# Kernel optimization log

Measured on AMD Instinct MI355X. Metric: run time of the kernel, lower is better.

Reference implementation:

```python
import jax, jax.numpy as jnp
import numpy as np
from jax import lax

SPLINE_ORDER = 3  # default in KANLinear


def make_grid(in_features, grid_size, order=SPLINE_ORDER):
    # grid_range = [-1, 1], extended by spline_order knots on each side
    h = 2.0 / grid_size
    g = jnp.arange(-order, grid_size + order + 1, dtype=jnp.float32) * h - 1.0
    return jnp.broadcast_to(g, (in_features, g.shape[0]))  # (in, G)


def b_splines(x, grid, order=SPLINE_ORDER):
    # x: (N, in), grid: (in, G). Cox-de Boor recursion.
    x = x[..., None]  # (N, in, 1)
    bases = ((x >= grid[:, :-1]) & (x < grid[:, 1:])).astype(x.dtype)
    for k in range(1, order + 1):
        bases = ((x - grid[:, : -(k + 1)]) / (grid[:, k:-1] - grid[:, : -(k + 1)]) * bases[..., :-1]
                 + (grid[:, k + 1:] - x) / (grid[:, k + 1:] - grid[:, 1:-k]) * bases[..., 1:])
    return bases  # (N, in, grid_size + order)


def kan_conv(x, base_w, spline_w, scaler, grid_size, kernel, pad):
    # x: (B, C, H, W); base_w: (n_convs, K); spline_w: (n_convs, K, grid_size+order); scaler: (n_convs, K)
    B, C, H, W = x.shape
    kh, kw = kernel
    K = kh * kw
    if K == 1:
        p = x.reshape(-1, 1)  # (B*C*H*W, 1)
        Ho, Wo = H, W
    else:
        # patches: (B, C*K, Ho, Wo), feature dim ordered channel-major then (kh, kw)
        patches = lax.conv_general_dilated_patches(x, (kh, kw), (1, 1), [(pad, pad), (pad, pad)])
        Ho, Wo = patches.shape[2], patches.shape[3]
        p = patches.reshape(B, C, K, Ho, Wo).transpose(0, 1, 3, 4, 2).reshape(-1, K)
    grid = make_grid(K, grid_size)
    bases = b_splines(p, grid)  # (N, K, coef) -- shared across all n_convs kernels
    base = jnp.einsum('ni,ki->nk', jax.nn.silu(p), base_w)
    spl = jnp.einsum('nic,kic->nk', bases, spline_w * scaler[..., None])
    n_convs = base_w.shape[0]
    # channel ordering: each input channel expanded into n_convs outputs (channel-major)
    out = (base + spl).reshape(B, C, Ho, Wo, n_convs).transpose(0, 1, 4, 2, 3)
    return out.reshape(B, C * n_convs, Ho, Wo)


def setup_inputs() -> dict:
    key = jax.random.key(0)
    ks = jax.random.split(key, 12)
    B, C, H, W = 4, 3, 256, 256
    coef3 = 3 + SPLINE_ORDER  # grid_size=3 -> 6 spline coefficients
    coef5 = 5 + SPLINE_ORDER  # grid_size=5 (default, kan_conv6) -> 8
    s9 = 1.0 / np.sqrt(9.0)
    return {
        'x': jax.random.normal(ks[0], (B, C, H, W), jnp.float32),
        'base_w1': jax.random.normal(ks[1], (2, 9), jnp.float32) * s9,
        'spline_w1': jax.random.normal(ks[2], (2, 9, coef3), jnp.float32) * 0.1,
        'scaler1': 1.0 + 0.1 * jax.random.normal(ks[3], (2, 9), jnp.float32),
        'base_w2': jax.random.normal(ks[4], (2, 9), jnp.float32) * s9,
        'spline_w2': jax.random.normal(ks[5], (2, 9, coef3), jnp.float32) * 0.1,
        'scaler2': 1.0 + 0.1 * jax.random.normal(ks[6], (2, 9), jnp.float32),
        'conv_w': jax.random.normal(ks[7], (3, 12, 1, 1), jnp.float32) * (1.0 / np.sqrt(12.0)),
        'conv_b': jax.random.normal(ks[8], (3,), jnp.float32) * 0.01,
        'base_w6': jax.random.normal(ks[9], (1, 1), jnp.float32),
        'spline_w6': jax.random.normal(ks[10], (1, 1, coef5), jnp.float32) * 0.1,
        'scaler6': 1.0 + 0.1 * jax.random.normal(ks[11], (1, 1), jnp.float32),
    }


def reference(x, base_w1, spline_w1, scaler1, base_w2, spline_w2, scaler2,
              conv_w, conv_b, base_w6, spline_w6, scaler6):
    x = kan_conv(x, base_w1, spline_w1, scaler1, grid_size=3, kernel=(3, 3), pad=1)   # (B,6,H,W)
    x = kan_conv(x, base_w2, spline_w2, scaler2, grid_size=3, kernel=(3, 3), pad=1)   # (B,12,H,W)
    x = jnp.einsum('bchw,oc->bohw', x, conv_w[:, :, 0, 0]) + conv_b[None, :, None, None]  # 1x1 conv -> (B,3,H,W)
    return kan_conv(x, base_w6, spline_w6, scaler6, grid_size=5, kernel=(1, 1), pad=0)  # (B,3,H,W)
```

## Files before the change

kernel.cpp:

```cpp
#include <hip/hip_runtime.h>
#include <hip/hip_fp16.h>

#define TILE 16
#define NT 768

typedef __fp16 h2f __attribute__((ext_vector_type(2)));

union H2U { h2f h; unsigned u; __half2 hh; };

__device__ __forceinline__ h2f u2h(unsigned u) { H2U t; t.u = u; return t.h; }

__device__ __forceinline__ unsigned pack_h2(float a, float b) {
    H2U t; t.hh = __halves2half2(__float2half_rn(a), __float2half_rn(b));
    return t.u;
}

__device__ __forceinline__ float fdot2(h2f a, h2f b, float acc) {
#if __has_builtin(__builtin_amdgcn_fdot2)
    return __builtin_amdgcn_fdot2(a, b, acc, false);
#else
    return acc + (float)a.x * (float)b.x + (float)a.y * (float)b.y;
#endif
}

struct Enc { float g, w; int si; };
__device__ __forceinline__ Enc kan_enc3(float v, float g0, float invh, float tmax) {
    Enc e;
    e.g = v / (1.0f + __expf(-v));
    float T = (v - g0) * invh;
    float U = (T >= 0.0f && T < tmax) ? T : -1.0f;
    float mf = floorf(U);
    e.w = U - mf;
    e.si = (int)mf + 1;
    return e;
}

__device__ __forceinline__ float poly_eval(float4 c, float w) {
    return ((c.w * w + c.z) * w + c.y) * w + c.x;
}

__device__ __forceinline__ float4 spline_poly(const float* __restrict__ sw, float sc,
                                              int ncoef, int si) {
    float4 v = make_float4(0.f, 0.f, 0.f, 0.f);
    if (si > 0) {
        int m = si - 1;
        float W[4];
        #pragma unroll
        for (int j = 0; j < 4; ++j) {
            int c = m - 3 + j;
            W[j] = (c >= 0 && c < ncoef) ? sw[c] * sc : 0.0f;
        }
        const float s6 = 1.0f / 6.0f;
        v.x = (W[0] + 4.0f * W[1] + W[2]) * s6;
        v.y = 3.0f * (W[2] - W[0]) * s6;
        v.z = (3.0f * W[0] - 6.0f * W[1] + 3.0f * W[2]) * s6;
        v.w = (W[3] - W[0] + 3.0f * (W[1] - W[2])) * s6;
    }
    return v;
}

__global__ __launch_bounds__(NT, 6) void ZS_MKAN_72121090834671_kernel(
    const float* __restrict__ x,
    const float* __restrict__ base_w1, const float* __restrict__ spline_w1,
    const float* __restrict__ scaler1,
    const float* __restrict__ base_w2, const float* __restrict__ spline_w2,
    const float* __restrict__ scaler2,
    const float* __restrict__ conv_w, const float* __restrict__ conv_b,
    const float* __restrict__ base_w6, const float* __restrict__ spline_w6,
    const float* __restrict__ scaler6,
    float* __restrict__ out)
{
    __shared__ float2  encXg[1200];
    __shared__ unsigned short encXs[1200];
    __shared__ float4  encYg[3][324];
    __shared__ ushort2 encYs[3][324];
    __shared__ uint4   coefH1[9][10];
    __shared__ uint4   coefH2[9][10];
    __shared__ float4  coef6[12];
    __shared__ float   sbw[2][18];
    __shared__ float   scw[36], scb[3];
    __shared__ float   sb6;
    __shared__ float   zpart[256][13];

    const int tid = threadIdx.x;
    const int tx0 = blockIdx.x * TILE;
    const int ty0 = blockIdx.y * TILE;
    const int b   = blockIdx.z;

    for (int e = tid; e < 180; e += NT) {
        int l = e / 90, r = e % 90, s = r / 10, si = r % 10;
        const float* sw  = l ? spline_w2 : spline_w1;
        const float* scl = l ? scaler2   : scaler1;
        float4 a = spline_poly(sw + s * 6,       scl[s],     6, si);
        float4 c = spline_poly(sw + (9 + s) * 6, scl[9 + s], 6, si);
        uint4 q;
        q.x = pack_h2(a.x, a.y); q.y = pack_h2(a.z, a.w);
        q.z = pack_h2(c.x, c.y); q.w = pack_h2(c.z, c.w);
        if (l) coefH2[s][si] = q; else coefH1[s][si] = q;
    }
    if (tid < 12) coef6[tid] = spline_poly(spline_w6, scaler6[0], 8, tid);
    if (tid < 18) { sbw[0][tid] = base_w1[tid]; sbw[1][tid] = base_w2[tid]; }
    if (tid < 36) scw[tid] = conv_w[tid];
    if (tid < 3)  scb[tid] = conv_b[tid];
    if (tid == 0) sb6 = base_w6[0];

    for (int i = tid; i < 1200; i += NT) {
        int c = i / 400, r = i % 400, ly = r / 20, lx = r % 20;
        int gy = ty0 - 2 + ly, gx = tx0 - 2 + lx;
        float v = 0.0f;
        if ((unsigned)gy < 256u && (unsigned)gx < 256u)
            v = x[((b * 3 + c) * 256 + gy) * 256 + gx];
        Enc e = kan_enc3(v, -3.0f, 1.5f, 9.0f);
        encXg[i] = make_float2(e.g, e.w);
        encXs[i] = (unsigned short)e.si;
    }
    __syncthreads();

    {
        float rb0[9], rb1[9];
        #pragma unroll
        for (int s = 0; s < 9; ++s) { rb0[s] = sbw[0][s]; rb1[s] = sbw[0][9 + s]; }
        for (int i = tid; i < 972; i += NT) {
            int c = i / 324, r = i % 324, ly = r / 18, lx = r % 18;
            float a0 = 0.0f, a1 = 0.0f;
            int base = c * 400 + ly * 20 + lx;
            #pragma unroll
            for (int s = 0; s < 9; ++s) {
                int p = base + (s / 3) * 20 + (s % 3);
                float2 gw = encXg[p];
                int si = encXs[p];
                uint4 q = coefH1[s][si];
                float w = gw.y, w2 = w * w;
                h2f p1 = __builtin_amdgcn_cvt_pkrtz(1.0f, w);
                h2f p2 = __builtin_amdgcn_cvt_pkrtz(w2, w2 * w);
                a0 += gw.x * rb0[s];
                a1 += gw.x * rb1[s];
                a0 = fdot2(u2h(q.x), p1, a0); a0 = fdot2(u2h(q.y), p2, a0);
                a1 = fdot2(u2h(q.z), p1, a1); a1 = fdot2(u2h(q.w), p2, a1);
            }
            int gy = ty0 - 1 + ly, gx = tx0 - 1 + lx;
            if (!((unsigned)gy < 256u && (unsigned)gx < 256u)) { a0 = 0.0f; a1 = 0.0f; }
            Enc e0 = kan_enc3(a0, -3.0f, 1.5f, 9.0f);
            Enc e1 = kan_enc3(a1, -3.0f, 1.5f, 9.0f);
            encYg[c][r] = make_float4(e0.g, e0.w, e1.g, e1.w);
            encYs[c][r] = make_ushort2((unsigned short)e0.si, (unsigned short)e1.si);
        }
    }
    __syncthreads();

    {
        const int pix = tid & 255;
        const int c   = tid >> 8;
        const int ly = pix >> 4, lx = pix & 15;
        float rb0[9], rb1[9];
        #pragma unroll
        for (int s = 0; s < 9; ++s) { rb0[s] = sbw[1][s]; rb1[s] = sbw[1][9 + s]; }
        const int rbase = ly * 18 + lx;
        float a00 = 0.0f, a01 = 0.0f, a10 = 0.0f, a11 = 0.0f;
        #pragma unroll
        for (int s = 0; s < 9; ++s) {
            int p = rbase + (s / 3) * 18 + (s % 3);
            float4 e = encYg[c][p];
            ushort2 ss = encYs[c][p];
            uint4 q0 = coefH2[s][ss.x];
            uint4 q1 = coefH2[s][ss.y];
            {
                float w = e.y, w2 = w * w;
                h2f p1 = __builtin_amdgcn_cvt_pkrtz(1.0f, w);
                h2f p2 = __builtin_amdgcn_cvt_pkrtz(w2, w2 * w);
                a00 += e.x * rb0[s];
                a01 += e.x * rb1[s];
                a00 = fdot2(u2h(q0.x), p1, a00); a00 = fdot2(u2h(q0.y), p2, a00);
                a01 = fdot2(u2h(q0.z), p1, a01); a01 = fdot2(u2h(q0.w), p2, a01);
            }
            {
                float w = e.w, w2 = w * w;
                h2f p1 = __builtin_amdgcn_cvt_pkrtz(1.0f, w);
                h2f p2 = __builtin_amdgcn_cvt_pkrtz(w2, w2 * w);
                a10 += e.z * rb0[s];
                a11 += e.z * rb1[s];
                a10 = fdot2(u2h(q1.x), p1, a10); a10 = fdot2(u2h(q1.y), p2, a10);
                a11 = fdot2(u2h(q1.z), p1, a11); a11 = fdot2(u2h(q1.w), p2, a11);
            }
        }
        zpart[pix][4 * c + 0] = a00;
        zpart[pix][4 * c + 1] = a01;
        zpart[pix][4 * c + 2] = a10;
        zpart[pix][4 * c + 3] = a11;
    }
    __syncthreads();

    if (tid < 256) {
        const int pix = tid;
        const int ly = pix >> 4, lx = pix & 15;
        const int gy = ty0 + ly, gx = tx0 + lx;
        float z[12];
        #pragma unroll
        for (int c = 0; c < 12; ++c) z[c] = zpart[pix][c];
        #pragma unroll
        for (int o = 0; o < 3; ++o) {
            float v = scb[o];
            #pragma unroll
            for (int c = 0; c < 12; ++c) v += scw[o * 12 + c] * z[c];
            Enc t = kan_enc3(v, -2.2f, 2.5f, 11.0f);
            out[((b * 3 + o) * 256 + gy) * 256 + gx] = t.g * sb6 + poly_eval(coef6[t.si], t.w);
        }
    }
}

extern "C" void kernel_launch(void* const* d_in, const int* in_sizes, int n_in,
                              void* d_out, int out_size, void* d_ws, size_t ws_size,
                              hipStream_t stream) {
    (void)in_sizes; (void)n_in; (void)d_ws; (void)ws_size; (void)out_size;
    const float* x         = (const float*)d_in[0];
    const float* base_w1   = (const float*)d_in[1];
    const float* spline_w1 = (const float*)d_in[2];
    const float* scaler1   = (const float*)d_in[3];
    const float* base_w2   = (const float*)d_in[4];
    const float* spline_w2 = (const float*)d_in[5];
    const float* scaler2   = (const float*)d_in[6];
    const float* conv_w    = (const float*)d_in[7];
    const float* conv_b    = (const float*)d_in[8];
    const float* base_w6   = (const float*)d_in[9];
    const float* spline_w6 = (const float*)d_in[10];
    const float* scaler6   = (const float*)d_in[11];
    float* out = (float*)d_out;

    dim3 grid(256 / TILE, 256 / TILE, 4);
    dim3 block(NT);
    ZS_MKAN_72121090834671_kernel<<<grid, block, 0, stream>>>(
        x, base_w1, spline_w1, scaler1, base_w2, spline_w2, scaler2,
        conv_w, conv_b, base_w6, spline_w6, scaler6, out);
}
```

Measured before the change: 24.00 us.

## Shrink block to 512 threads, alias zpart over encX, split stage-2 work

Lowers the block size from 768 to 512 threads and raises the launch-bounds occupancy hint to 8. Shared memory is cut by letting the stage-3 partial-sum buffer reuse the space of the first-layer input encoding, which is dead by then. Stage 2 is reorganised so each work item handles one of the two output halves, spread over 1536 items with a strided loop. The setup loads are spread across different thread ranges, and an extra barrier is added after them. The aim is more resident blocks per CU and lower register pressure, at the cost of more loop iterations and an added sync.

```diff
diff --git a/kernel.cpp b/kernel.cpp
--- a/kernel.cpp
+++ b/kernel.cpp
@@ -2,7 +2,7 @@
 #include <hip/hip_fp16.h>
 
 #define TILE 16
-#define NT 768
+#define NT 512
 
 typedef __fp16 h2f __attribute__((ext_vector_type(2)));
 
@@ -59,7 +59,7 @@
     return v;
 }
 
-__global__ __launch_bounds__(NT, 6) void ZS_MKAN_72121090834671_kernel(
+__global__ __launch_bounds__(NT, 8) void ZS_MKAN_72121090834671_kernel(
     const float* __restrict__ x,
     const float* __restrict__ base_w1, const float* __restrict__ spline_w1,
     const float* __restrict__ scaler1,
@@ -70,8 +70,11 @@
     const float* __restrict__ scaler6,
     float* __restrict__ out)
 {
-    __shared__ float2  encXg[1200];
-    __shared__ unsigned short encXs[1200];
+    __shared__ __align__(16) char xz[13312];
+    float2*         encXg = (float2*)xz;
+    unsigned short* encXs = (unsigned short*)(xz + 9600);
+    float*          zpart = (float*)xz;
+
     __shared__ float4  encYg[3][324];
     __shared__ ushort2 encYs[3][324];
     __shared__ uint4   coefH1[9][10];
@@ -80,14 +83,14 @@
     __shared__ float   sbw[2][18];
     __shared__ float   scw[36], scb[3];
     __shared__ float   sb6;
-    __shared__ float   zpart[256][13];
 
     const int tid = threadIdx.x;
     const int tx0 = blockIdx.x * TILE;
     const int ty0 = blockIdx.y * TILE;
     const int b   = blockIdx.z;
 
-    for (int e = tid; e < 180; e += NT) {
+    if (tid < 180) {
+        int e = tid;
         int l = e / 90, r = e % 90, s = r / 10, si = r % 10;
         const float* sw  = l ? spline_w2 : spline_w1;
         const float* scl = l ? scaler2   : scaler1;
@@ -97,13 +100,18 @@
         q.x = pack_h2(a.x, a.y); q.y = pack_h2(a.z, a.w);
         q.z = pack_h2(c.x, c.y); q.w = pack_h2(c.z, c.w);
         if (l) coefH2[s][si] = q; else coefH1[s][si] = q;
-    }
-    if (tid < 12) coef6[tid] = spline_poly(spline_w6, scaler6[0], 8, tid);
-    if (tid < 18) { sbw[0][tid] = base_w1[tid]; sbw[1][tid] = base_w2[tid]; }
-    if (tid < 36) scw[tid] = conv_w[tid];
-    if (tid < 3)  scb[tid] = conv_b[tid];
-    if (tid == 0) sb6 = base_w6[0];
-
+    } else if (tid < 192) {
+        coef6[tid - 180] = spline_poly(spline_w6, scaler6[0], 8, tid - 180);
+    } else if (tid < 228) {
+        int i = tid - 192;
+        scw[i] = conv_w[i];
+        if (i < 18) { sbw[0][i] = base_w1[i]; sbw[1][i] = base_w2[i]; }
+        if (i < 3)  scb[i] = conv_b[i];
+        if (i == 0) sb6 = base_w6[0];
+    }
+    __syncthreads();
+
+    #pragma unroll 1
     for (int i = tid; i < 1200; i += NT) {
         int c = i / 400, r = i % 400, ly = r / 20, lx = r % 20;
         int gy = ty0 - 2 + ly, gx = tx0 - 2 + lx;
@@ -120,6 +128,7 @@
         float rb0[9], rb1[9];
         #pragma unroll
         for (int s = 0; s < 9; ++s) { rb0[s] = sbw[0][s]; rb1[s] = sbw[0][9 + s]; }
+        #pragma unroll 1
         for (int i = tid; i < 972; i += NT) {
             int c = i / 324, r = i % 324, ly = r / 18, lx = r % 18;
             float a0 = 0.0f, a1 = 0.0f;
@@ -149,54 +158,45 @@
     __syncthreads();
 
     {
-        const int pix = tid & 255;
-        const int c   = tid >> 8;
-        const int ly = pix >> 4, lx = pix & 15;
         float rb0[9], rb1[9];
         #pragma unroll
         for (int s = 0; s < 9; ++s) { rb0[s] = sbw[1][s]; rb1[s] = sbw[1][9 + s]; }
-        const int rbase = ly * 18 + lx;
-        float a00 = 0.0f, a01 = 0.0f, a10 = 0.0f, a11 = 0.0f;
-        #pragma unroll
-        for (int s = 0; s < 9; ++s) {
-            int p = rbase + (s / 3) * 18 + (s % 3);
-            float4 e = encYg[c][p];
-            ushort2 ss = encYs[c][p];
-            uint4 q0 = coefH2[s][ss.x];
-            uint4 q1 = coefH2[s][ss.y];
-            {
-                float w = e.y, w2 = w * w;
+        #pragma unroll 1
+        for (int u = tid; u < 1536; u += NT) {
+            const int pix = u & 255;
+            const int ch  = u >> 8;
+            const int c   = ch >> 1, h = ch & 1;
+            const int rbase = (pix >> 4) * 18 + (pix & 15);
+            float a0 = 0.0f, a1 = 0.0f;
+            #pragma unroll
+            for (int s = 0; s < 9; ++s) {
+                int p = rbase + (s / 3) * 18 + (s % 3);
+                float4 e = encYg[c][p];
+                ushort2 ss = encYs[c][p];
+                float g  = h ? e.z : e.x;
+                float w  = h ? e.w : e.y;
+                int   si = h ? ss.y : ss.x;
+                uint4 q = coefH2[s][si];
+                float w2 = w * w;
                 h2f p1 = __builtin_amdgcn_cvt_pkrtz(1.0f, w);
                 h2f p2 = __builtin_amdgcn_cvt_pkrtz(w2, w2 * w);
-                a00 += e.x * rb0[s];
-                a01 += e.x * rb1[s];
-                a00 = fdot2(u2h(q0.x), p1, a00); a00 = fdot2(u2h(q0.y), p2, a00);
-                a01 = fdot2(u2h(q0.z), p1, a01); a01 = fdot2(u2h(q0.w), p2, a01);
+                a0 += g * rb0[s];
+                a1 += g * rb1[s];
+                a0 = fdot2(u2h(q.x), p1, a0); a0 = fdot2(u2h(q.y), p2, a0);
+                a1 = fdot2(u2h(q.z), p1, a1); a1 = fdot2(u2h(q.w), p2, a1);
             }
-            {
-                float w = e.w, w2 = w * w;
-                h2f p1 = __builtin_amdgcn_cvt_pkrtz(1.0f, w);
-                h2f p2 = __builtin_amdgcn_cvt_pkrtz(w2, w2 * w);
-                a10 += e.z * rb0[s];
-                a11 += e.z * rb1[s];
-                a10 = fdot2(u2h(q1.x), p1, a10); a10 = fdot2(u2h(q1.y), p2, a10);
-                a11 = fdot2(u2h(q1.z), p1, a11); a11 = fdot2(u2h(q1.w), p2, a11);
-            }
-        }
-        zpart[pix][4 * c + 0] = a00;
-        zpart[pix][4 * c + 1] = a01;
-        zpart[pix][4 * c + 2] = a10;
-        zpart[pix][4 * c + 3] = a11;
+            zpart[pix * 13 + 4 * c + 2 * h + 0] = a0;
+            zpart[pix * 13 + 4 * c + 2 * h + 1] = a1;
+        }
     }
     __syncthreads();
 
     if (tid < 256) {
         const int pix = tid;
-        const int ly = pix >> 4, lx = pix & 15;
-        const int gy = ty0 + ly, gx = tx0 + lx;
+        const int gy = ty0 + (pix >> 4), gx = tx0 + (pix & 15);
         float z[12];
         #pragma unroll
-        for (int c = 0; c < 12; ++c) z[c] = zpart[pix][c];
+        for (int c = 0; c < 12; ++c) z[c] = zpart[pix * 13 + c];
         #pragma unroll
         for (int o = 0; o < 3; ++o) {
             float v = scb[o];
```

Result: slower. 25.71 us (+7.1%).
